# Kernel tuning notes

Hardware: AMD Instinct MI355X
Metric: run time of the kernel (lower is better)

The kernel has to match this reference:

```python
import jax, jax.numpy as jnp
import numpy as np

EMB = 1024
FFN = 4096
H = 16
HD = EMB // H
EPS = 1e-6
SLOPE = 0.01


def leaky_relu(x):
    return jnp.where(x >= 0, x, SLOPE * x)


def layer_norm(x, g, b):
    mu = jnp.mean(x, axis=-1, keepdims=True)
    var = jnp.mean((x - mu) ** 2, axis=-1, keepdims=True)
    return (x - mu) * jax.lax.rsqrt(var + EPS) * g + b


def setup_inputs() -> dict:
    key = jax.random.key(0)
    ks = jax.random.split(key, 16)
    B, N = 2, 2048
    x = jax.random.normal(ks[0], (B, N, EMB), dtype=jnp.float32)

    def lin(k, fan_in, fan_out, kaiming_normal):
        kw, kb = jax.random.split(k)
        gain = float(np.sqrt(2.0 / (1.0 + SLOPE ** 2)))
        if kaiming_normal:
            W = jax.random.normal(kw, (fan_out, fan_in)) * (gain / np.sqrt(fan_in))
        else:
            bound = gain * np.sqrt(3.0 / fan_in)
            W = jax.random.uniform(kw, (fan_out, fan_in), minval=-bound, maxval=bound)
        b = jax.random.normal(kb, (fan_out,)) * 1e-6
        return W.astype(jnp.float32), b.astype(jnp.float32)

    Wq, bq = lin(ks[1], EMB, EMB, True)
    Wk, bk = lin(ks[2], EMB, EMB, True)
    Wv, bv = lin(ks[3], EMB, EMB, True)
    Wo, bo = lin(ks[4], EMB, EMB, True)
    W1, b1 = lin(ks[5], EMB, FFN, False)
    W2, b2 = lin(ks[6], FFN, EMB, False)
    return {
        "x": x,
        "ln1_g": jnp.ones((EMB,)), "ln1_b": jnp.zeros((EMB,)),
        "ln2_g": jnp.ones((EMB,)), "ln2_b": jnp.zeros((EMB,)),
        "Wq": Wq, "bq": bq, "Wk": Wk, "bk": bk, "Wv": Wv, "bv": bv,
        "Wo": Wo, "bo": bo, "W1": W1, "b1": b1, "W2": W2, "b2": b2,
    }


def reference(x, ln1_g, ln1_b, ln2_g, ln2_b, Wq, bq, Wk, bk, Wv, bv, Wo, bo, W1, b1, W2, b2):
    B, N, _ = x.shape
    h = x
    xn = layer_norm(x, ln1_g, ln1_b)
    # QKV projections, split heads: [B, H, N, HD]
    def heads(t):
        return t.reshape(B, N, H, HD).transpose(0, 2, 1, 3)
    q = heads(xn @ Wq.T + bq)
    k = heads(xn @ Wk.T + bk)
    v = heads(xn @ Wv.T + bv)
    scores = jnp.einsum('bhnd,bhmd->bhnm', q, k) / jnp.sqrt(jnp.float32(HD))
    probs = leaky_relu(scores)  # non-softmax attention
    ctx = jnp.einsum('bhnm,bhmd->bhnd', probs, v)
    ctx = ctx.transpose(0, 2, 1, 3).reshape(B, N, EMB)
    attn_out = ctx @ Wo.T + bo
    x = attn_out + h
    h = x
    xn = layer_norm(x, ln2_g, ln2_b)
    ff = leaky_relu(xn @ W1.T + b1) @ W2.T + b2
    return ff + h
```

## Files before the change

kernel.cpp:

```cpp
#include <hip/hip_runtime.h>
#include <hip/hip_bf16.h>


typedef unsigned short u16;
typedef __bf16 bf16x8 __attribute__((ext_vector_type(8)));
typedef float f32x4 __attribute__((ext_vector_type(4)));
typedef unsigned short u16x8 __attribute__((ext_vector_type(8)));

typedef const __attribute__((address_space(1))) void* as1cv;
typedef __attribute__((address_space(3))) void* as3v;

#define MFMA16(a, b, c) __builtin_amdgcn_mfma_f32_16x16x32_bf16((a), (b), (c), 0, 0, 0)
#define GLL16(g, l) __builtin_amdgcn_global_load_lds((as1cv)(g), (as3v)(l), 16, 0, 0)

__device__ __forceinline__ u16 f2bf(float f) {
  unsigned u = __builtin_bit_cast(unsigned, f);
  u += 0x7fffu + ((u >> 16) & 1u);
  return (u16)(u >> 16);
}
__device__ __forceinline__ float lrelu(float v) { return v >= 0.f ? v : 0.01f * v; }

__global__ __launch_bounds__(256) void cvt6(
    const float* __restrict__ p0, const float* __restrict__ p1,
    const float* __restrict__ p2, const float* __restrict__ p3,
    const float* __restrict__ p4, const float* __restrict__ p5,
    u16* __restrict__ o0, u16* __restrict__ o1, u16* __restrict__ o2,
    u16* __restrict__ o3, u16* __restrict__ o4, u16* __restrict__ o5)
{
  int i = blockIdx.x * 256 + threadIdx.x;
  const float* src; u16* dst; int off;
  if (i < 4 * 131072) {
    int s = i >> 17; off = i & 131071;
    src = (s == 0) ? p0 : (s == 1) ? p1 : (s == 2) ? p2 : p3;
    dst = (s == 0) ? o0 : (s == 1) ? o1 : (s == 2) ? o2 : o3;
  } else {
    int j = i - 4 * 131072;
    int s = j >> 19; off = j & 524287;
    src = s ? p5 : p4;
    dst = s ? o5 : o4;
  }
  const float4* s4 = (const float4*)src;
  float4 a = s4[(size_t)off * 2], b = s4[(size_t)off * 2 + 1];
  u16x8 o = { f2bf(a.x), f2bf(a.y), f2bf(a.z), f2bf(a.w),
              f2bf(b.x), f2bf(b.y), f2bf(b.z), f2bf(b.w) };
  *(u16x8*)(dst + (size_t)off * 8) = o;
}

__global__ __launch_bounds__(256) void ln_k(
    const float* __restrict__ x, const float* __restrict__ g,
    const float* __restrict__ bb, u16* __restrict__ out)
{
  const int tid = threadIdx.x;
  const int row = blockIdx.x;
  const float4* xr = (const float4*)(x + (size_t)row * 1024);
  float4 v = xr[tid];
  float s  = v.x + v.y + v.z + v.w;
  float s2 = v.x*v.x + v.y*v.y + v.z*v.z + v.w*v.w;
#pragma unroll
  for (int o = 32; o > 0; o >>= 1) { s += __shfl_down(s, o, 64); s2 += __shfl_down(s2, o, 64); }
  __shared__ float sh[8];
  if ((tid & 63) == 0) { sh[tid >> 6] = s; sh[4 + (tid >> 6)] = s2; }
  __syncthreads();
  s  = sh[0] + sh[1] + sh[2] + sh[3];
  s2 = sh[4] + sh[5] + sh[6] + sh[7];
  float mu  = s * (1.0f / 1024.0f);
  float var = s2 * (1.0f / 1024.0f) - mu * mu;
  float rs  = rsqrtf(var + 1e-6f);
  float4 gv = ((const float4*)g)[tid];
  float4 bv = ((const float4*)bb)[tid];
  ushort4 o;
  o.x = f2bf((v.x - mu) * rs * gv.x + bv.x);
  o.y = f2bf((v.y - mu) * rs * gv.y + bv.y);
  o.z = f2bf((v.z - mu) * rs * gv.z + bv.z);
  o.w = f2bf((v.w - mu) * rs * gv.w + bv.w);
  ((ushort4*)out)[(size_t)row * 256 + tid] = o;
}

__device__ __forceinline__ void gemm_core128(
    const u16* __restrict__ A, const u16* __restrict__ W, int K,
    int row0, int wrow0, u16* lsA, u16* lsB, f32x4 (&acc)[4][4])
{
  const int tid  = threadIdx.x;
  const int lane = tid & 63, wave = tid >> 6;
  const int wr = wave >> 1, wc = wave & 1;
  const int lr = lane & 15, lg = lane >> 4;

  const u16* ga0 = A + (size_t)(row0 + (tid >> 2)) * K + (tid & 3) * 8;
  const u16* ga1 = ga0 + (size_t)64 * K;
  const u16* gb0 = W + (size_t)(wrow0 + (tid >> 2)) * K + (tid & 3) * 8;
  const u16* gb1 = gb0 + (size_t)64 * K;
  u16* la0 = lsA + tid * 8;
  u16* la1 = lsA + 2048 + tid * 8;
  u16* lb0 = lsB + tid * 8;
  u16* lb1 = lsB + 2048 + tid * 8;

  for (int k0 = 0; k0 < K; k0 += 32) {
    GLL16(ga0, la0); GLL16(ga1, la1);
    GLL16(gb0, lb0); GLL16(gb1, lb1);
    ga0 += 32; ga1 += 32; gb0 += 32; gb1 += 32;
    __syncthreads();
    bf16x8 av[4], bv[4];
#pragma unroll
    for (int mi = 0; mi < 4; mi++)
      av[mi] = *reinterpret_cast<const bf16x8*>(lsA + (wr * 64 + mi * 16 + lr) * 32 + lg * 8);
#pragma unroll
    for (int ni = 0; ni < 4; ni++)
      bv[ni] = *reinterpret_cast<const bf16x8*>(lsB + (wc * 64 + ni * 16 + lr) * 32 + lg * 8);
#pragma unroll
    for (int mi = 0; mi < 4; mi++)
#pragma unroll
      for (int ni = 0; ni < 4; ni++)
        acc[mi][ni] = MFMA16(av[mi], bv[ni], acc[mi][ni]);
    __syncthreads();
  }
}

__global__ __launch_bounds__(256, 2) void gemm_qkv(
    const u16* __restrict__ xn,
    const u16* __restrict__ Wq, const u16* __restrict__ Wk, const u16* __restrict__ Wv,
    const float* __restrict__ bq, const float* __restrict__ bk, const float* __restrict__ bv,
    u16* __restrict__ qb, u16* __restrict__ kb, u16* __restrict__ vtb)
{
  __shared__ u16 lsA[128 * 32];
  __shared__ u16 lsB[128 * 32];
  const int mt = blockIdx.x / 24, nt = blockIdx.x % 24;
  const int row0 = mt * 128, col0 = nt * 128;
  const int sel = col0 >> 10, c0 = col0 & 1023;
  const u16* W = (sel == 0) ? Wq : (sel == 1) ? Wk : Wv;
  const float* bias = (sel == 0) ? bq : (sel == 1) ? bk : bv;

  f32x4 acc[4][4];
  f32x4 z = {0.f, 0.f, 0.f, 0.f};
#pragma unroll
  for (int mi = 0; mi < 4; mi++)
#pragma unroll
    for (int ni = 0; ni < 4; ni++) acc[mi][ni] = z;

  gemm_core128(xn, W, 1024, row0, c0, lsA, lsB, acc);

  const int lane = threadIdx.x & 63, wave = threadIdx.x >> 6;
  const int wr = wave >> 1, wc = wave & 1;
  const int lr = lane & 15, lg = lane >> 4;
#pragma unroll
  for (int ni = 0; ni < 4; ni++) {
    int c = c0 + wc * 64 + ni * 16 + lr;
    float bsv = bias[c];
    int h = c >> 6, hd = c & 63;
#pragma unroll
    for (int mi = 0; mi < 4; mi++) {
      int rbase = row0 + wr * 64 + mi * 16 + lg * 4;
      int b = rbase >> 11;
      int n = rbase & 2047;
      if (sel < 2) {
        u16* dst = (sel == 0) ? qb : kb;
        size_t base = ((size_t)(b * 16 + h) * 2048 + n) * 64 + hd;
#pragma unroll
        for (int r = 0; r < 4; r++)
          dst[base + (size_t)r * 64] = f2bf(acc[mi][ni][r] + bsv);
      } else {
        size_t base = ((size_t)((b * 16 + h) * 64 + hd)) * 2048 + n;
        ushort4 o;
        o.x = f2bf(acc[mi][ni][0] + bsv);
        o.y = f2bf(acc[mi][ni][1] + bsv);
        o.z = f2bf(acc[mi][ni][2] + bsv);
        o.w = f2bf(acc[mi][ni][3] + bsv);
        *(ushort4*)(vtb + base) = o;
      }
    }
  }
}

template <int EPI>
__global__ __launch_bounds__(256, 2) void gemm128(
    const u16* __restrict__ A, const u16* __restrict__ W,
    const float* __restrict__ bias, float* __restrict__ outf,
    u16* __restrict__ outh, const float* __restrict__ extra,
    int K, int nTiles)
{
  __shared__ u16 lsA[128 * 32];
  __shared__ u16 lsB[128 * 32];
  const int mt = blockIdx.x / nTiles, nt = blockIdx.x % nTiles;
  const int row0 = mt * 128, col0 = nt * 128;

  f32x4 acc[4][4];
  f32x4 z = {0.f, 0.f, 0.f, 0.f};
#pragma unroll
  for (int mi = 0; mi < 4; mi++)
#pragma unroll
    for (int ni = 0; ni < 4; ni++) acc[mi][ni] = z;

  gemm_core128(A, W, K, row0, col0, lsA, lsB, acc);

  const int N = nTiles * 128;
  const int lane = threadIdx.x & 63, wave = threadIdx.x >> 6;
  const int wr = wave >> 1, wc = wave & 1;
  const int lr = lane & 15, lg = lane >> 4;
#pragma unroll
  for (int ni = 0; ni < 4; ni++) {
    int col = col0 + wc * 64 + ni * 16 + lr;
    float bsv = bias[col];
#pragma unroll
    for (int mi = 0; mi < 4; mi++) {
      int rbase = row0 + wr * 64 + mi * 16 + lg * 4;
#pragma unroll
      for (int r = 0; r < 4; r++) {
        float v = acc[mi][ni][r] + bsv;
        size_t idx = (size_t)(rbase + r) * N + col;
        if (EPI == 0) {
          outf[idx] = v + extra[idx];
        } else {
          outh[idx] = f2bf(lrelu(v));
        }
      }
    }
  }
}

__device__ __forceinline__ int swz(int row, int col) {
  return row * 64 + (col ^ ((row & 7) << 3));
}

__global__ __launch_bounds__(256, 3) void attn_k(
    const u16* __restrict__ qb, const u16* __restrict__ kb,
    const u16* __restrict__ vtb, u16* __restrict__ ctx)
{
  __shared__ u16 lq[128 * 64];
  __shared__ u16 lk[64 * 64];
  __shared__ u16 lv[64 * 64];
  __shared__ u16 lp[128 * 64];

  const int tid = threadIdx.x;
  const int lane = tid & 63, wave = tid >> 6;
  const int wr = wave >> 1, wc = wave & 1;
  const int lr = lane & 15, lg = lane >> 4;
  const int bh = blockIdx.x >> 4, qt = blockIdx.x & 15;
  const int n0 = qt * 128;
  const u16* qh = qb + (size_t)bh * 2048 * 64;
  const u16* kh = kb + (size_t)bh * 2048 * 64;
  const u16* vh = vtb + (size_t)bh * 64 * 2048;

  {
    int r = tid >> 3, kk = (tid & 7) * 8;
#pragma unroll
    for (int j = 0; j < 4; j++)
      *(u16x8*)(lq + swz(j * 32 + r, kk)) =
          *(const u16x8*)(qh + (size_t)(n0 + j * 32 + r) * 64 + kk);
  }

  f32x4 z = {0.f, 0.f, 0.f, 0.f};
  f32x4 cacc[4][2];
#pragma unroll
  for (int mi = 0; mi < 4; mi++)
#pragma unroll
    for (int ni = 0; ni < 2; ni++) cacc[mi][ni] = z;

  for (int kt = 0; kt < 32; kt++) {
    {
      int r = tid >> 3, kk = (tid & 7) * 8;
#pragma unroll
      for (int j = 0; j < 2; j++) {
        *(u16x8*)(lk + swz(j * 32 + r, kk)) =
            *(const u16x8*)(kh + (size_t)(kt * 64 + j * 32 + r) * 64 + kk);
        *(u16x8*)(lv + swz(j * 32 + r, kk)) =
            *(const u16x8*)(vh + (size_t)(j * 32 + r) * 2048 + kt * 64 + kk);
      }
    }
    __syncthreads();

    f32x4 sacc[4][2];
#pragma unroll
    for (int mi = 0; mi < 4; mi++)
#pragma unroll
      for (int ni = 0; ni < 2; ni++) sacc[mi][ni] = z;
#pragma unroll
    for (int ks = 0; ks < 2; ks++) {
      bf16x8 aq[4], bk8[2];
#pragma unroll
      for (int mi = 0; mi < 4; mi++)
        aq[mi] = *reinterpret_cast<const bf16x8*>(lq + swz(wr * 64 + mi * 16 + lr, ks * 32 + lg * 8));
#pragma unroll
      for (int ni = 0; ni < 2; ni++)
        bk8[ni] = *reinterpret_cast<const bf16x8*>(lk + swz(wc * 32 + ni * 16 + lr, ks * 32 + lg * 8));
#pragma unroll
      for (int mi = 0; mi < 4; mi++)
#pragma unroll
        for (int ni = 0; ni < 2; ni++)
          sacc[mi][ni] = MFMA16(aq[mi], bk8[ni], sacc[mi][ni]);
    }
#pragma unroll
    for (int mi = 0; mi < 4; mi++)
#pragma unroll
      for (int ni = 0; ni < 2; ni++)
#pragma unroll
        for (int r = 0; r < 4; r++) {
          float v = lrelu(sacc[mi][ni][r] * 0.125f);
          int i = wr * 64 + mi * 16 + lg * 4 + r;
          int j = wc * 32 + ni * 16 + lr;
          lp[swz(i, j)] = f2bf(v);
        }
    __syncthreads();

#pragma unroll
    for (int js = 0; js < 2; js++) {
      bf16x8 pa[4], vb[2];
#pragma unroll
      for (int mi = 0; mi < 4; mi++)
        pa[mi] = *reinterpret_cast<const bf16x8*>(lp + swz(wr * 64 + mi * 16 + lr, js * 32 + lg * 8));
#pragma unroll
      for (int ni = 0; ni < 2; ni++)
        vb[ni] = *reinterpret_cast<const bf16x8*>(lv + swz(wc * 32 + ni * 16 + lr, js * 32 + lg * 8));
#pragma unroll
      for (int mi = 0; mi < 4; mi++)
#pragma unroll
        for (int ni = 0; ni < 2; ni++)
          cacc[mi][ni] = MFMA16(pa[mi], vb[ni], cacc[mi][ni]);
    }
    __syncthreads();
  }

  const int b = bh >> 4, h = bh & 15;
#pragma unroll
  for (int mi = 0; mi < 4; mi++)
#pragma unroll
    for (int ni = 0; ni < 2; ni++)
#pragma unroll
      for (int r = 0; r < 4; r++) {
        int n = n0 + wr * 64 + mi * 16 + lg * 4 + r;
        int d = wc * 32 + ni * 16 + lr;
        ctx[((size_t)(b * 2048 + n)) * 1024 + h * 64 + d] = f2bf(cacc[mi][ni][r]);
      }
}

extern "C" void kernel_launch(void* const* d_in, const int* in_sizes, int n_in,
                              void* d_out, int out_size, void* d_ws, size_t ws_size,
                              hipStream_t stream) {
  (void)in_sizes; (void)n_in; (void)out_size; (void)ws_size;
  const float* x    = (const float*)d_in[0];
  const float* ln1g = (const float*)d_in[1];
  const float* ln1b = (const float*)d_in[2];
  const float* ln2g = (const float*)d_in[3];
  const float* ln2b = (const float*)d_in[4];
  const float* Wq = (const float*)d_in[5];  const float* bq = (const float*)d_in[6];
  const float* Wk = (const float*)d_in[7];  const float* bk = (const float*)d_in[8];
  const float* Wv = (const float*)d_in[9];  const float* bv = (const float*)d_in[10];
  const float* Wo = (const float*)d_in[11]; const float* bo = (const float*)d_in[12];
  const float* W1 = (const float*)d_in[13]; const float* b1 = (const float*)d_in[14];
  const float* W2 = (const float*)d_in[15]; const float* b2 = (const float*)d_in[16];

  char* ws = (char*)d_ws;
  u16*   WqB  = (u16*)(ws + ((size_t)0 << 20));
  u16*   WkB  = (u16*)(ws + ((size_t)2 << 20));
  u16*   WvB  = (u16*)(ws + ((size_t)4 << 20));
  u16*   WoB  = (u16*)(ws + ((size_t)6 << 20));
  u16*   W1B  = (u16*)(ws + ((size_t)8 << 20));
  u16*   W2B  = (u16*)(ws + ((size_t)16 << 20));
  u16*   xn1  = (u16*)(ws + ((size_t)24 << 20));
  u16*   qb   = (u16*)(ws + ((size_t)32 << 20));
  u16*   kb   = (u16*)(ws + ((size_t)40 << 20));
  u16*   vtb  = (u16*)(ws + ((size_t)48 << 20));
  u16*   ctxb = (u16*)(ws + ((size_t)56 << 20));
  float* x2   = (float*)(ws + ((size_t)64 << 20));
  u16*   xn2  = (u16*)(ws + ((size_t)80 << 20));
  u16*   ff1  = (u16*)(ws + ((size_t)88 << 20));

  dim3 blk(256);

  cvt6<<<dim3(6144), blk, 0, stream>>>(Wq, Wk, Wv, Wo, W1, W2,
                                       WqB, WkB, WvB, WoB, W1B, W2B);
  ln_k<<<dim3(4096), blk, 0, stream>>>(x, ln1g, ln1b, xn1);
  gemm_qkv<<<dim3(768), blk, 0, stream>>>(xn1, WqB, WkB, WvB, bq, bk, bv,
                                          qb, kb, vtb);
  attn_k<<<dim3(512), blk, 0, stream>>>(qb, kb, vtb, ctxb);
  gemm128<0><<<dim3(256), blk, 0, stream>>>(ctxb, WoB, bo, x2, (u16*)nullptr, x,
                                            1024, 8);
  ln_k<<<dim3(4096), blk, 0, stream>>>(x2, ln2g, ln2b, xn2);
  gemm128<1><<<dim3(1024), blk, 0, stream>>>(xn2, W1B, b1, (float*)nullptr, ff1,
                                             (const float*)nullptr, 1024, 32);
  gemm128<0><<<dim3(256), blk, 0, stream>>>(ff1, W2B, b2, (float*)d_out,
                                            (u16*)nullptr, x2, 4096, 8);
}
```

Baseline: 404.6 us.

## Double-buffer GEMM LDS, add XCD-aware block remap, split-K FFN2 with reduce

The shared GEMM core now double-buffers its LDS tiles so the global-to-LDS loads for the next K step are issued before the MFMAs on the current step, and the occupancy hint rises from 2 to 4 blocks per CU. All GEMMs and the attention kernel remap block IDs so consecutive tiles land on the same XCD. The FFN2 GEMM, which previously launched only 256 blocks with K=4096, is split into four K chunks over 1024 blocks that write bf16 partials, followed by a reduce kernel that adds bias and residual. The split-K path adds extra memory traffic for the partials, and storing them in bf16 loses some precision. The doubled LDS footprint may also keep the requested occupancy from being reached.

```diff
diff --git a/kernel.cpp b/kernel.cpp
--- a/kernel.cpp
+++ b/kernel.cpp
@@ -18,7 +18,15 @@
   u += 0x7fffu + ((u >> 16) & 1u);
   return (u16)(u >> 16);
 }
+__device__ __forceinline__ float bf2f(u16 u) {
+  return __builtin_bit_cast(float, ((unsigned)u) << 16);
+}
 __device__ __forceinline__ float lrelu(float v) { return v >= 0.f ? v : 0.01f * v; }
+
+__device__ __forceinline__ int xcds(int bid, int nwg) {
+  int cpx = nwg >> 3;
+  return (bid & 7) * cpx + (bid >> 3);
+}
 
 __global__ __launch_bounds__(256) void cvt6(
     const float* __restrict__ p0, const float* __restrict__ p1,
@@ -77,7 +85,8 @@
 }
 
 __device__ __forceinline__ void gemm_core128(
-    const u16* __restrict__ A, const u16* __restrict__ W, int K,
+    const u16* __restrict__ A, const u16* __restrict__ W,
+    int kstride, int klen,
     int row0, int wrow0, u16* lsA, u16* lsB, f32x4 (&acc)[4][4])
 {
   const int tid  = threadIdx.x;
@@ -85,45 +94,58 @@
   const int wr = wave >> 1, wc = wave & 1;
   const int lr = lane & 15, lg = lane >> 4;
 
-  const u16* ga0 = A + (size_t)(row0 + (tid >> 2)) * K + (tid & 3) * 8;
-  const u16* ga1 = ga0 + (size_t)64 * K;
-  const u16* gb0 = W + (size_t)(wrow0 + (tid >> 2)) * K + (tid & 3) * 8;
-  const u16* gb1 = gb0 + (size_t)64 * K;
-  u16* la0 = lsA + tid * 8;
-  u16* la1 = lsA + 2048 + tid * 8;
-  u16* lb0 = lsB + tid * 8;
-  u16* lb1 = lsB + 2048 + tid * 8;
-
-  for (int k0 = 0; k0 < K; k0 += 32) {
-    GLL16(ga0, la0); GLL16(ga1, la1);
-    GLL16(gb0, lb0); GLL16(gb1, lb1);
-    ga0 += 32; ga1 += 32; gb0 += 32; gb1 += 32;
-    __syncthreads();
+  const u16* ga0 = A + (size_t)(row0 + (tid >> 2)) * kstride + (tid & 3) * 8;
+  const u16* ga1 = ga0 + (size_t)64 * kstride;
+  const u16* gb0 = W + (size_t)(wrow0 + (tid >> 2)) * kstride + (tid & 3) * 8;
+  const u16* gb1 = gb0 + (size_t)64 * kstride;
+  u16* la = lsA + tid * 8;
+  u16* lb = lsB + tid * 8;
+
+  GLL16(ga0, la); GLL16(ga1, la + 2048);
+  GLL16(gb0, lb); GLL16(gb1, lb + 2048);
+  ga0 += 32; ga1 += 32; gb0 += 32; gb1 += 32;
+  __syncthreads();
+
+  const int nsteps = klen >> 5;
+  int cur = 0;
+  for (int t = 0; t < nsteps; t++) {
+    int nxt = cur ^ 1;
+    if (t + 1 < nsteps) {
+      GLL16(ga0, la + nxt * 4096);
+      GLL16(ga1, la + nxt * 4096 + 2048);
+      GLL16(gb0, lb + nxt * 4096);
+      GLL16(gb1, lb + nxt * 4096 + 2048);
+      ga0 += 32; ga1 += 32; gb0 += 32; gb1 += 32;
+    }
+    const u16* cA = lsA + cur * 4096;
+    const u16* cB = lsB + cur * 4096;
     bf16x8 av[4], bv[4];
 #pragma unroll
     for (int mi = 0; mi < 4; mi++)
-      av[mi] = *reinterpret_cast<const bf16x8*>(lsA + (wr * 64 + mi * 16 + lr) * 32 + lg * 8);
+      av[mi] = *reinterpret_cast<const bf16x8*>(cA + (wr * 64 + mi * 16 + lr) * 32 + lg * 8);
 #pragma unroll
     for (int ni = 0; ni < 4; ni++)
-      bv[ni] = *reinterpret_cast<const bf16x8*>(lsB + (wc * 64 + ni * 16 + lr) * 32 + lg * 8);
+      bv[ni] = *reinterpret_cast<const bf16x8*>(cB + (wc * 64 + ni * 16 + lr) * 32 + lg * 8);
 #pragma unroll
     for (int mi = 0; mi < 4; mi++)
 #pragma unroll
       for (int ni = 0; ni < 4; ni++)
         acc[mi][ni] = MFMA16(av[mi], bv[ni], acc[mi][ni]);
     __syncthreads();
-  }
-}
-
-__global__ __launch_bounds__(256, 2) void gemm_qkv(
+    cur = nxt;
+  }
+}
+
+__global__ __launch_bounds__(256, 4) void gemm_qkv(
     const u16* __restrict__ xn,
     const u16* __restrict__ Wq, const u16* __restrict__ Wk, const u16* __restrict__ Wv,
     const float* __restrict__ bq, const float* __restrict__ bk, const float* __restrict__ bv,
     u16* __restrict__ qb, u16* __restrict__ kb, u16* __restrict__ vtb)
 {
-  __shared__ u16 lsA[128 * 32];
-  __shared__ u16 lsB[128 * 32];
-  const int mt = blockIdx.x / 24, nt = blockIdx.x % 24;
+  __shared__ u16 lsA[2 * 128 * 32];
+  __shared__ u16 lsB[2 * 128 * 32];
+  const int wid = xcds(blockIdx.x, 768);
+  const int mt = wid / 24, nt = wid % 24;
   const int row0 = mt * 128, col0 = nt * 128;
   const int sel = col0 >> 10, c0 = col0 & 1023;
   const u16* W = (sel == 0) ? Wq : (sel == 1) ? Wk : Wv;
@@ -136,7 +158,7 @@
 #pragma unroll
     for (int ni = 0; ni < 4; ni++) acc[mi][ni] = z;
 
-  gemm_core128(xn, W, 1024, row0, c0, lsA, lsB, acc);
+  gemm_core128(xn, W, 1024, 1024, row0, c0, lsA, lsB, acc);
 
   const int lane = threadIdx.x & 63, wave = threadIdx.x >> 6;
   const int wr = wave >> 1, wc = wave & 1;
@@ -171,15 +193,16 @@
 }
 
 template <int EPI>
-__global__ __launch_bounds__(256, 2) void gemm128(
+__global__ __launch_bounds__(256, 4) void gemm128(
     const u16* __restrict__ A, const u16* __restrict__ W,
     const float* __restrict__ bias, float* __restrict__ outf,
     u16* __restrict__ outh, const float* __restrict__ extra,
-    int K, int nTiles)
-{
-  __shared__ u16 lsA[128 * 32];
-  __shared__ u16 lsB[128 * 32];
-  const int mt = blockIdx.x / nTiles, nt = blockIdx.x % nTiles;
+    int K, int nTiles, int nwg)
+{
+  __shared__ u16 lsA[2 * 128 * 32];
+  __shared__ u16 lsB[2 * 128 * 32];
+  const int wid = xcds(blockIdx.x, nwg);
+  const int mt = wid / nTiles, nt = wid % nTiles;
   const int row0 = mt * 128, col0 = nt * 128;
 
   f32x4 acc[4][4];
@@ -189,7 +212,7 @@
 #pragma unroll
     for (int ni = 0; ni < 4; ni++) acc[mi][ni] = z;
 
-  gemm_core128(A, W, K, row0, col0, lsA, lsB, acc);
+  gemm_core128(A, W, K, K, row0, col0, lsA, lsB, acc);
 
   const int N = nTiles * 128;
   const int lane = threadIdx.x & 63, wave = threadIdx.x >> 6;
@@ -216,6 +239,64 @@
   }
 }
 
+__global__ __launch_bounds__(256, 4) void gemm_ffn2(
+    const u16* __restrict__ A, const u16* __restrict__ W,
+    u16* __restrict__ pout)
+{
+  __shared__ u16 lsA[2 * 128 * 32];
+  __shared__ u16 lsB[2 * 128 * 32];
+  const int wid = xcds(blockIdx.x, 1024);
+  const int chunk = wid >> 8, rem = wid & 255;
+  const int mt = rem >> 3, nt = rem & 7;
+  const int row0 = mt * 128, col0 = nt * 128;
+
+  f32x4 acc[4][4];
+  f32x4 z = {0.f, 0.f, 0.f, 0.f};
+#pragma unroll
+  for (int mi = 0; mi < 4; mi++)
+#pragma unroll
+    for (int ni = 0; ni < 4; ni++) acc[mi][ni] = z;
+
+  gemm_core128(A + chunk * 1024, W + chunk * 1024, 4096, 1024,
+               row0, col0, lsA, lsB, acc);
+
+  u16* out = pout + (size_t)chunk * (4096 * 1024);
+  const int lane = threadIdx.x & 63, wave = threadIdx.x >> 6;
+  const int wr = wave >> 1, wc = wave & 1;
+  const int lr = lane & 15, lg = lane >> 4;
+#pragma unroll
+  for (int ni = 0; ni < 4; ni++) {
+    int col = col0 + wc * 64 + ni * 16 + lr;
+#pragma unroll
+    for (int mi = 0; mi < 4; mi++) {
+      int rbase = row0 + wr * 64 + mi * 16 + lg * 4;
+#pragma unroll
+      for (int r = 0; r < 4; r++)
+        out[(size_t)(rbase + r) * 1024 + col] = f2bf(acc[mi][ni][r]);
+    }
+  }
+}
+
+__global__ __launch_bounds__(256) void reduce_ffn2(
+    const u16* __restrict__ p, const float* __restrict__ b2,
+    const float* __restrict__ x2, float* __restrict__ out)
+{
+  size_t i = ((size_t)blockIdx.x * 256 + threadIdx.x) * 4;
+  int col = (int)(i & 1023);
+  ushort4 a0 = *(const ushort4*)(p + i);
+  ushort4 a1 = *(const ushort4*)(p + (size_t)(4096 * 1024) + i);
+  ushort4 a2 = *(const ushort4*)(p + (size_t)(2 * 4096 * 1024) + i);
+  ushort4 a3 = *(const ushort4*)(p + (size_t)(3 * 4096 * 1024) + i);
+  float4 bv = *(const float4*)(b2 + col);
+  float4 xv = *(const float4*)(x2 + i);
+  float4 r;
+  r.x = bf2f(a0.x) + bf2f(a1.x) + bf2f(a2.x) + bf2f(a3.x) + bv.x + xv.x;
+  r.y = bf2f(a0.y) + bf2f(a1.y) + bf2f(a2.y) + bf2f(a3.y) + bv.y + xv.y;
+  r.z = bf2f(a0.z) + bf2f(a1.z) + bf2f(a2.z) + bf2f(a3.z) + bv.z + xv.z;
+  r.w = bf2f(a0.w) + bf2f(a1.w) + bf2f(a2.w) + bf2f(a3.w) + bv.w + xv.w;
+  *(float4*)(out + i) = r;
+}
+
 __device__ __forceinline__ int swz(int row, int col) {
   return row * 64 + (col ^ ((row & 7) << 3));
 }
@@ -233,7 +314,8 @@
   const int lane = tid & 63, wave = tid >> 6;
   const int wr = wave >> 1, wc = wave & 1;
   const int lr = lane & 15, lg = lane >> 4;
-  const int bh = blockIdx.x >> 4, qt = blockIdx.x & 15;
+  const int wid = xcds(blockIdx.x, 512);
+  const int bh = wid >> 4, qt = wid & 15;
   const int n0 = qt * 128;
   const u16* qh = qb + (size_t)bh * 2048 * 64;
   const u16* kh = kb + (size_t)bh * 2048 * 64;
@@ -362,6 +444,7 @@
   float* x2   = (float*)(ws + ((size_t)64 << 20));
   u16*   xn2  = (u16*)(ws + ((size_t)80 << 20));
   u16*   ff1  = (u16*)(ws + ((size_t)88 << 20));
+  u16*   pF2  = (u16*)(ws + ((size_t)24 << 20));
 
   dim3 blk(256);
 
@@ -372,10 +455,10 @@
                                           qb, kb, vtb);
   attn_k<<<dim3(512), blk, 0, stream>>>(qb, kb, vtb, ctxb);
   gemm128<0><<<dim3(256), blk, 0, stream>>>(ctxb, WoB, bo, x2, (u16*)nullptr, x,
-                                            1024, 8);
+                                            1024, 8, 256);
   ln_k<<<dim3(4096), blk, 0, stream>>>(x2, ln2g, ln2b, xn2);
   gemm128<1><<<dim3(1024), blk, 0, stream>>>(xn2, W1B, b1, (float*)nullptr, ff1,
-                                             (const float*)nullptr, 1024, 32);
-  gemm128<0><<<dim3(256), blk, 0, stream>>>(ff1, W2B, b2, (float*)d_out,
-                                            (u16*)nullptr, x2, 4096, 8);
-}
+                                             (const float*)nullptr, 1024, 32, 1024);
+  gemm_ffn2<<<dim3(1024), blk, 0, stream>>>(ff1, W2B, pF2);
+  reduce_ffn2<<<dim3(4096), blk, 0, stream>>>(pF2, b2, x2, (float*)d_out);
+}
```

Result: faster. 353.4 us (-12.7%).
